# Optimization experiments

Hardware: AMD Instinct MI355X
Metric: run time of the kernel (lower is better)

## Reference

```python
import jax, jax.numpy as jnp
import numpy as np

N_NODES = 50000
N_EDGES = 800000
IN_C = 128
HID = 64
HEADS = 4
OUT_C = 32
NEG_SLOPE = 0.2
EPS = 1e-16


def _gat_conv(x, edge_index, W, att_src, att_dst, bias, heads, out_c, concat):
    # PyG GATConv (eval mode, add_self_loops=True).
    N = x.shape[0]
    # append self loops
    loops = jnp.arange(N, dtype=edge_index.dtype)
    src = jnp.concatenate([edge_index[0], loops])
    dst = jnp.concatenate([edge_index[1], loops])
    h = (x @ W).reshape(N, heads, out_c)                      # [N,H,C]
    a_src = jnp.sum(h * att_src, axis=-1)                     # [N,H]
    a_dst = jnp.sum(h * att_dst, axis=-1)                     # [N,H]
    alpha = a_src[src] + a_dst[dst]                           # [E,H]
    alpha = jnp.where(alpha >= 0, alpha, NEG_SLOPE * alpha)   # leaky_relu
    amax = jax.ops.segment_max(alpha, dst, num_segments=N)    # [N,H]
    ex = jnp.exp(alpha - amax[dst])
    denom = jax.ops.segment_sum(ex, dst, num_segments=N)      # [N,H]
    coef = ex / (denom[dst] + EPS)                            # [E,H]
    msg = h[src] * coef[:, :, None]                           # [E,H,C]
    out = jax.ops.segment_sum(msg, dst, num_segments=N)       # [N,H,C]
    if concat:
        out = out.reshape(N, heads * out_c)
    else:
        out = out.mean(axis=1)
    return out + bias


def setup_inputs() -> dict:
    key = jax.random.key(0)
    ks = jax.random.split(key, 12)
    x = jax.random.normal(ks[0], (N_NODES, IN_C), dtype=jnp.float32)
    edge_index = jax.random.randint(ks[1], (2, N_EDGES), 0, N_NODES, dtype=jnp.int64)
    s1 = 1.0 / np.sqrt(IN_C)
    s2 = 1.0 / np.sqrt(HID * HEADS)
    W1 = jax.random.uniform(ks[2], (IN_C, HEADS * HID), jnp.float32, -s1, s1)
    att_src1 = jax.random.uniform(ks[3], (HEADS, HID), jnp.float32, -s1, s1)
    att_dst1 = jax.random.uniform(ks[4], (HEADS, HID), jnp.float32, -s1, s1)
    b1 = jnp.zeros((HEADS * HID,), jnp.float32)
    W2 = jax.random.uniform(ks[5], (HEADS * HID, OUT_C), jnp.float32, -s2, s2)
    att_src2 = jax.random.uniform(ks[6], (1, OUT_C), jnp.float32, -s2, s2)
    att_dst2 = jax.random.uniform(ks[7], (1, OUT_C), jnp.float32, -s2, s2)
    b2 = jnp.zeros((OUT_C,), jnp.float32)
    return {"x": x, "edge_index": edge_index, "W1": W1, "att_src1": att_src1,
            "att_dst1": att_dst1, "b1": b1, "W2": W2, "att_src2": att_src2,
            "att_dst2": att_dst2, "b2": b2}


def reference(x, edge_index, W1, att_src1, att_dst1, b1, W2, att_src2, att_dst2, b2):
    h = _gat_conv(x, edge_index, W1, att_src1, att_dst1, b1, HEADS, HID, concat=True)
    h = jax.nn.elu(h)
    out = _gat_conv(h, edge_index, W2, att_src2, att_dst2, b2, 1, OUT_C, concat=False)
    return out
```

## Files before the change

### kernel.cpp

```cpp
#include <hip/hip_runtime.h>

#define NN 50000
#define NE 800000
#define INC 128
#define HIDC 64
#define HEADS 4
#define C1 256
#define OUTC 32
#define NEG 0.2f
#define EPSV 1e-16f
#define SLOT_CAP 56

#define NB_CASTX 3125
#define NB_ZERO  196
#define NB_W1T   128
#define NB_W2T   32
#define NB_PREP  (NB_CASTX + NB_ZERO + NB_W1T + NB_W2T)
#define EB2      3125
#define NB_G1S   782
#define NB_G1    (NB_G1S * 4)
#define NB_GS    (EB2 + NB_G1)

#define CURS  0
#define ASRC1 50000
#define ADST1 250000
#define ASRC2 450000
#define ADST2 500000
#define SLOTS 550000
#define W1T   3350000
#define W2T   3366384
#define XBF   3370480
#define H1B   6570480
#define H2B   12970480
#define H3OFF 19370480
#define WS_NEED_FLOATS 20170480ull

typedef __attribute__((ext_vector_type(8))) short short8v;
typedef __attribute__((ext_vector_type(4))) float floatx4;

__device__ __forceinline__ unsigned short f2bf(float f) {
    unsigned u = __float_as_uint(f);
    unsigned r = (u + 0x7fffu + ((u >> 16) & 1u)) >> 16;
    return (unsigned short)r;
}
__device__ __forceinline__ float bf2f(unsigned short s) {
    return __uint_as_float(((unsigned)s) << 16);
}
__device__ __forceinline__ float lrelu(float v) { return v >= 0.f ? v : NEG * v; }

__global__ __launch_bounds__(256) void prep(const float* __restrict__ x,
                                            const float* __restrict__ W1,
                                            const float* __restrict__ W2,
                                            unsigned short* __restrict__ xbf,
                                            unsigned short* __restrict__ w1t,
                                            unsigned short* __restrict__ w2t,
                                            int* __restrict__ curs) {
    const int bid = blockIdx.x, tid = threadIdx.x;
    if (bid < NB_CASTX) {
        int i = bid * 256 + tid;
        float4 v0 = ((const float4*)x)[i * 2];
        float4 v1 = ((const float4*)x)[i * 2 + 1];
        short8v o;
        o[0] = (short)f2bf(v0.x); o[1] = (short)f2bf(v0.y);
        o[2] = (short)f2bf(v0.z); o[3] = (short)f2bf(v0.w);
        o[4] = (short)f2bf(v1.x); o[5] = (short)f2bf(v1.y);
        o[6] = (short)f2bf(v1.z); o[7] = (short)f2bf(v1.w);
        *(short8v*)(xbf + (size_t)i * 8) = o;
    } else if (bid < NB_CASTX + NB_ZERO) {
        int i = (bid - NB_CASTX) * 256 + tid;
        if (i < NN) curs[i] = 0;
    } else if (bid < NB_CASTX + NB_ZERO + NB_W1T) {
        int i = (bid - NB_CASTX - NB_ZERO) * 256 + tid;
        int n = i >> 7, k = i & 127;
        w1t[(size_t)n * INC + k] = f2bf(W1[(size_t)k * C1 + n]);
    } else {
        int i = (bid - NB_CASTX - NB_ZERO - NB_W1T) * 256 + tid;
        int n = i >> 8, k = i & 255;
        w2t[(size_t)n * C1 + k] = f2bf(W2[(size_t)k * OUTC + n]);
    }
}

__global__ __launch_bounds__(256) void gemm1_scatter(const unsigned short* __restrict__ xbf,
                                                     const unsigned short* __restrict__ w1t,
                                                     const float* __restrict__ att_src,
                                                     const float* __restrict__ att_dst,
                                                     const int* __restrict__ ei,
                                                     unsigned short* __restrict__ h1b,
                                                     float* __restrict__ a_src,
                                                     float* __restrict__ a_dst,
                                                     int* __restrict__ curs,
                                                     int* __restrict__ slots) {
    const int bid = blockIdx.x;
    if (bid < EB2) {
        int e = bid * 256 + threadIdx.x;
        if (e < NE) {
            int s = ei[e], d = ei[NE + e];
            int pos = atomicAdd(&curs[d], 1);
            if (pos < SLOT_CAP) slots[(size_t)d * SLOT_CAP + pos] = s;
        }
        return;
    }
    const int b2 = bid - EB2;
    const int strip = b2 % NB_G1S;
    const int by = b2 / NB_G1S;
    const int tid = threadIdx.x;
    const int w = tid >> 6, lane = tid & 63;
    const int l15 = lane & 15, kg = lane >> 4;
    const int mb = strip * 64 + w * 16;
    const int nb = by * 64;
    int ar = mb + l15; if (ar >= NN) ar = NN - 1;

    short8v a[4];
    #pragma unroll
    for (int ks = 0; ks < 4; ++ks)
        a[ks] = *(const short8v*)(xbf + (size_t)ar * INC + ks * 32 + kg * 8);

    short8v b[4][4];
    #pragma unroll
    for (int nt = 0; nt < 4; ++nt) {
        int nc = nb + nt * 16 + l15;
        #pragma unroll
        for (int ks = 0; ks < 4; ++ks)
            b[ks][nt] = *(const short8v*)(w1t + (size_t)nc * INC + ks * 32 + kg * 8);
    }

    floatx4 acc[4] = {{0.f,0.f,0.f,0.f},{0.f,0.f,0.f,0.f},{0.f,0.f,0.f,0.f},{0.f,0.f,0.f,0.f}};
    #pragma unroll
    for (int ks = 0; ks < 4; ++ks)
        #pragma unroll
        for (int nt = 0; nt < 4; ++nt)
            acc[nt] = __builtin_amdgcn_mfma_f32_16x16x32_bf16(a[ks], b[ks][nt], acc[nt], 0, 0, 0);

    #pragma unroll
    for (int nt = 0; nt < 4; ++nt)
        #pragma unroll
        for (int j = 0; j < 4; ++j) {
            int r = mb + kg * 4 + j;
            if (r < NN) h1b[(size_t)r * C1 + nb + nt * 16 + l15] = f2bf(acc[nt][j]);
        }

    float ws_[4], wd_[4];
    #pragma unroll
    for (int nt = 0; nt < 4; ++nt) {
        ws_[nt] = att_src[nb + nt * 16 + l15];
        wd_[nt] = att_dst[nb + nt * 16 + l15];
    }
    #pragma unroll
    for (int j = 0; j < 4; ++j) {
        float ps = acc[0][j] * ws_[0] + acc[1][j] * ws_[1] + acc[2][j] * ws_[2] + acc[3][j] * ws_[3];
        float pd = acc[0][j] * wd_[0] + acc[1][j] * wd_[1] + acc[2][j] * wd_[2] + acc[3][j] * wd_[3];
        #pragma unroll
        for (int m = 8; m; m >>= 1) {
            ps += __shfl_xor(ps, m);
            pd += __shfl_xor(pd, m);
        }
        int r = mb + kg * 4 + j;
        if (l15 == 0 && r < NN) {
            a_src[r * 4 + by] = ps;
            a_dst[r * 4 + by] = pd;
        }
    }
}

__global__ __launch_bounds__(256) void node1(const unsigned short* __restrict__ h1b,
                                             const int* __restrict__ curs,
                                             const int* __restrict__ slots,
                                             const float* __restrict__ a_src,
                                             const float* __restrict__ a_dst,
                                             const float* __restrict__ b1,
                                             unsigned short* __restrict__ h2b) {
    int wave = threadIdx.x >> 6, lane = threadIdx.x & 63;
    int n = blockIdx.x * 4 + wave;
    if (n >= NN) return;
    int h = lane >> 4;
    int cnt = curs[n]; if (cnt > SLOT_CAP) cnt = SLOT_CAP;
    const int* sl = slots + (size_t)n * SLOT_CAP;
    float adh = a_dst[n * 4 + h];
    float a0 = 0.f, a1 = 0.f, a2 = 0.f, a3 = 0.f, den = 0.f;
    {
        float e = __expf(lrelu(a_src[n * 4 + h] + adh));
        den += e;
        uint2 rv = *(const uint2*)(h1b + (size_t)n * C1 + lane * 4);
        a0 += bf2f((unsigned short)(rv.x & 0xffff)) * e;
        a1 += bf2f((unsigned short)(rv.x >> 16)) * e;
        a2 += bf2f((unsigned short)(rv.y & 0xffff)) * e;
        a3 += bf2f((unsigned short)(rv.y >> 16)) * e;
    }
    int p = 0;
    for (; p + 7 < cnt; p += 8) {
        int sA[8];
        #pragma unroll
        for (int j = 0; j < 8; ++j) sA[j] = sl[p + j];
        uint2 rA[8];
        #pragma unroll
        for (int j = 0; j < 8; ++j) rA[j] = *(const uint2*)(h1b + (size_t)sA[j] * C1 + lane * 4);
        float eA[8];
        #pragma unroll
        for (int j = 0; j < 8; ++j) eA[j] = __expf(lrelu(a_src[sA[j] * 4 + h] + adh));
        #pragma unroll
        for (int j = 0; j < 8; ++j) {
            den += eA[j];
            a0 += bf2f((unsigned short)(rA[j].x & 0xffff)) * eA[j];
            a1 += bf2f((unsigned short)(rA[j].x >> 16)) * eA[j];
            a2 += bf2f((unsigned short)(rA[j].y & 0xffff)) * eA[j];
            a3 += bf2f((unsigned short)(rA[j].y >> 16)) * eA[j];
        }
    }
    for (; p + 3 < cnt; p += 4) {
        int sA[4];
        #pragma unroll
        for (int j = 0; j < 4; ++j) sA[j] = sl[p + j];
        uint2 rA[4];
        #pragma unroll
        for (int j = 0; j < 4; ++j) rA[j] = *(const uint2*)(h1b + (size_t)sA[j] * C1 + lane * 4);
        float eA[4];
        #pragma unroll
        for (int j = 0; j < 4; ++j) eA[j] = __expf(lrelu(a_src[sA[j] * 4 + h] + adh));
        #pragma unroll
        for (int j = 0; j < 4; ++j) {
            den += eA[j];
            a0 += bf2f((unsigned short)(rA[j].x & 0xffff)) * eA[j];
            a1 += bf2f((unsigned short)(rA[j].x >> 16)) * eA[j];
            a2 += bf2f((unsigned short)(rA[j].y & 0xffff)) * eA[j];
            a3 += bf2f((unsigned short)(rA[j].y >> 16)) * eA[j];
        }
    }
    for (; p < cnt; ++p) {
        int s = sl[p];
        float e = __expf(lrelu(a_src[s * 4 + h] + adh));
        den += e;
        uint2 rv = *(const uint2*)(h1b + (size_t)s * C1 + lane * 4);
        a0 += bf2f((unsigned short)(rv.x & 0xffff)) * e;
        a1 += bf2f((unsigned short)(rv.x >> 16)) * e;
        a2 += bf2f((unsigned short)(rv.y & 0xffff)) * e;
        a3 += bf2f((unsigned short)(rv.y >> 16)) * e;
    }
    float inv = 1.f / (den + EPSV);
    float4 bb = *(const float4*)(b1 + lane * 4);
    float o0 = a0 * inv + bb.x;
    float o1 = a1 * inv + bb.y;
    float o2 = a2 * inv + bb.z;
    float o3 = a3 * inv + bb.w;
    o0 = o0 > 0.f ? o0 : __expf(o0) - 1.f;
    o1 = o1 > 0.f ? o1 : __expf(o1) - 1.f;
    o2 = o2 > 0.f ? o2 : __expf(o2) - 1.f;
    o3 = o3 > 0.f ? o3 : __expf(o3) - 1.f;
    uint2 ov;
    ov.x = (unsigned)f2bf(o0) | ((unsigned)f2bf(o1) << 16);
    ov.y = (unsigned)f2bf(o2) | ((unsigned)f2bf(o3) << 16);
    *(uint2*)(h2b + (size_t)n * C1 + lane * 4) = ov;
}

__global__ __launch_bounds__(256) void gemm2_mfma(const unsigned short* __restrict__ h2b,
                                                  const unsigned short* __restrict__ w2t,
                                                  const float* __restrict__ att_src,
                                                  const float* __restrict__ att_dst,
                                                  unsigned short* __restrict__ h3b,
                                                  float* __restrict__ a_src,
                                                  float* __restrict__ a_dst) {
    const int tid = threadIdx.x;
    const int w = tid >> 6, lane = tid & 63;
    const int l15 = lane & 15, kg = lane >> 4;
    const int mb = blockIdx.x * 64 + w * 16;
    int ar = mb + l15; if (ar >= NN) ar = NN - 1;

    short8v a[8];
    #pragma unroll
    for (int ks = 0; ks < 8; ++ks)
        a[ks] = *(const short8v*)(h2b + (size_t)ar * C1 + ks * 32 + kg * 8);

    short8v b[8][2];
    #pragma unroll
    for (int nt = 0; nt < 2; ++nt) {
        int nc = nt * 16 + l15;
        #pragma unroll
        for (int ks = 0; ks < 8; ++ks)
            b[ks][nt] = *(const short8v*)(w2t + (size_t)nc * C1 + ks * 32 + kg * 8);
    }

    floatx4 acc[2] = {{0.f,0.f,0.f,0.f},{0.f,0.f,0.f,0.f}};
    #pragma unroll
    for (int ks = 0; ks < 8; ++ks)
        #pragma unroll
        for (int nt = 0; nt < 2; ++nt)
            acc[nt] = __builtin_amdgcn_mfma_f32_16x16x32_bf16(a[ks], b[ks][nt], acc[nt], 0, 0, 0);

    #pragma unroll
    for (int nt = 0; nt < 2; ++nt)
        #pragma unroll
        for (int j = 0; j < 4; ++j) {
            int r = mb + kg * 4 + j;
            if (r < NN) h3b[(size_t)r * OUTC + nt * 16 + l15] = f2bf(acc[nt][j]);
        }

    float ws0 = att_src[l15], ws1 = att_src[16 + l15];
    float wd0 = att_dst[l15], wd1 = att_dst[16 + l15];
    #pragma unroll
    for (int j = 0; j < 4; ++j) {
        float ps = acc[0][j] * ws0 + acc[1][j] * ws1;
        float pd = acc[0][j] * wd0 + acc[1][j] * wd1;
        #pragma unroll
        for (int m = 8; m; m >>= 1) {
            ps += __shfl_xor(ps, m);
            pd += __shfl_xor(pd, m);
        }
        int r = mb + kg * 4 + j;
        if (l15 == 0 && r < NN) {
            a_src[r] = ps;
            a_dst[r] = pd;
        }
    }
}

__global__ __launch_bounds__(256) void node2(const unsigned short* __restrict__ h3b,
                                             const int* __restrict__ curs,
                                             const int* __restrict__ slots,
                                             const float* __restrict__ a_src,
                                             const float* __restrict__ a_dst,
                                             const float* __restrict__ b2,
                                             float* __restrict__ out) {
    int wave = threadIdx.x >> 6, lane = threadIdx.x & 63;
    int half = lane >> 5, c = lane & 31;
    int n = blockIdx.x * 8 + wave * 2 + half;
    if (n >= NN) return;
    int cnt = curs[n]; if (cnt > SLOT_CAP) cnt = SLOT_CAP;
    const int* sl = slots + (size_t)n * SLOT_CAP;
    float adn = a_dst[n];
    float acc = 0.f, den = 0.f;
    {
        float e = __expf(lrelu(a_src[n] + adn));
        den += e;
        acc += bf2f(h3b[(size_t)n * OUTC + c]) * e;
    }
    int p = 0;
    for (; p + 3 < cnt; p += 4) {
        int s0 = sl[p], s1 = sl[p + 1], s2 = sl[p + 2], s3 = sl[p + 3];
        float g0 = bf2f(h3b[(size_t)s0 * OUTC + c]);
        float g1 = bf2f(h3b[(size_t)s1 * OUTC + c]);
        float g2 = bf2f(h3b[(size_t)s2 * OUTC + c]);
        float g3 = bf2f(h3b[(size_t)s3 * OUTC + c]);
        float e0 = __expf(lrelu(a_src[s0] + adn));
        float e1 = __expf(lrelu(a_src[s1] + adn));
        float e2 = __expf(lrelu(a_src[s2] + adn));
        float e3 = __expf(lrelu(a_src[s3] + adn));
        den += e0 + e1 + e2 + e3;
        acc += g0 * e0 + g1 * e1 + g2 * e2 + g3 * e3;
    }
    for (; p < cnt; ++p) {
        int s = sl[p];
        float e = __expf(lrelu(a_src[s] + adn));
        den += e;
        acc += bf2f(h3b[(size_t)s * OUTC + c]) * e;
    }
    out[(size_t)n * OUTC + c] = acc / (den + EPSV) + b2[c];
}

extern "C" void kernel_launch(void* const* d_in, const int* in_sizes, int n_in,
                              void* d_out, int out_size, void* d_ws, size_t ws_size,
                              hipStream_t stream) {
    if (ws_size < WS_NEED_FLOATS * 4ull) return;

    const float* x        = (const float*)d_in[0];
    const int* ei         = (const int*)d_in[1];
    const float* W1       = (const float*)d_in[2];
    const float* att_src1 = (const float*)d_in[3];
    const float* att_dst1 = (const float*)d_in[4];
    const float* b1       = (const float*)d_in[5];
    const float* W2       = (const float*)d_in[6];
    const float* att_src2 = (const float*)d_in[7];
    const float* att_dst2 = (const float*)d_in[8];
    const float* b2       = (const float*)d_in[9];
    float* out = (float*)d_out;
    float* ws  = (float*)d_ws;
    int*   wsi = (int*)d_ws;

    int*   curs   = wsi + CURS;
    float* a_src1 = ws + ASRC1;
    float* a_dst1 = ws + ADST1;
    float* a_src2 = ws + ASRC2;
    float* a_dst2 = ws + ADST2;
    int*   slots  = wsi + SLOTS;
    unsigned short* w1t = (unsigned short*)(ws + W1T);
    unsigned short* w2t = (unsigned short*)(ws + W2T);
    unsigned short* xbf = (unsigned short*)(ws + XBF);
    unsigned short* h1b = (unsigned short*)(ws + H1B);
    unsigned short* h2b = (unsigned short*)(ws + H2B);
    unsigned short* h3b = (unsigned short*)(ws + H3OFF);

    hipLaunchKernelGGL(prep, dim3(NB_PREP), dim3(256), 0, stream,
                       x, W1, W2, xbf, w1t, w2t, curs);
    hipLaunchKernelGGL(gemm1_scatter, dim3(NB_GS), dim3(256), 0, stream,
                       xbf, w1t, att_src1, att_dst1, ei, h1b, a_src1, a_dst1, curs, slots);
    hipLaunchKernelGGL(node1, dim3((NN + 3) / 4), dim3(256), 0, stream,
                       h1b, curs, slots, a_src1, a_dst1, b1, h2b);
    hipLaunchKernelGGL(gemm2_mfma, dim3((NN + 63) / 64), dim3(256), 0, stream,
                       h2b, w2t, att_src2, att_dst2, h3b, a_src2, a_dst2);
    hipLaunchKernelGGL(node2, dim3((NN + 7) / 8), dim3(256), 0, stream,
                       h3b, curs, slots, a_src2, a_dst2, b2, out);
}
```

Baseline: 199.6 us.

## Split edge scatter by destination half to overlap with node aggregation

The edge-to-slot scatter is split by destination node index. Edges into the low half are bucketed alongside the first GEMM, and edges into the high half are bucketed in a new kernel that also aggregates the low-half nodes. The high-half nodes are then aggregated in a separate kernel. The aim is to overlap scatter atomics with GEMM and aggregation work, at the cost of one extra launch and reading the edge index twice.

```diff
diff --git a/kernel.cpp b/kernel.cpp
--- a/kernel.cpp
+++ b/kernel.cpp
@@ -10,6 +10,7 @@
 #define NEG 0.2f
 #define EPSV 1e-16f
 #define SLOT_CAP 56
+#define HSPLIT 25000
 
 #define NB_CASTX 3125
 #define NB_ZERO  196
@@ -20,6 +21,8 @@
 #define NB_G1S   782
 #define NB_G1    (NB_G1S * 4)
 #define NB_GS    (EB2 + NB_G1)
+#define NB_N1H   6250
+#define NB_SN    (EB2 + NB_N1H)
 
 #define CURS  0
 #define ASRC1 50000
@@ -80,6 +83,93 @@
     }
 }
 
+__device__ __forceinline__ void node1_body(int n, int lane,
+                                           const unsigned short* __restrict__ h1b,
+                                           const int* __restrict__ curs,
+                                           const int* __restrict__ slots,
+                                           const float* __restrict__ a_src,
+                                           const float* __restrict__ a_dst,
+                                           const float* __restrict__ b1,
+                                           unsigned short* __restrict__ h2b) {
+    int h = lane >> 4;
+    int cnt = curs[n]; if (cnt > SLOT_CAP) cnt = SLOT_CAP;
+    const int* sl = slots + (size_t)n * SLOT_CAP;
+    float adh = a_dst[n * 4 + h];
+    float a0 = 0.f, a1 = 0.f, a2 = 0.f, a3 = 0.f, den = 0.f;
+    {
+        float e = __expf(lrelu(a_src[n * 4 + h] + adh));
+        den += e;
+        uint2 rv = *(const uint2*)(h1b + (size_t)n * C1 + lane * 4);
+        a0 += bf2f((unsigned short)(rv.x & 0xffff)) * e;
+        a1 += bf2f((unsigned short)(rv.x >> 16)) * e;
+        a2 += bf2f((unsigned short)(rv.y & 0xffff)) * e;
+        a3 += bf2f((unsigned short)(rv.y >> 16)) * e;
+    }
+    int p = 0;
+    for (; p + 7 < cnt; p += 8) {
+        int sA[8];
+        #pragma unroll
+        for (int j = 0; j < 8; ++j) sA[j] = sl[p + j];
+        uint2 rA[8];
+        #pragma unroll
+        for (int j = 0; j < 8; ++j) rA[j] = *(const uint2*)(h1b + (size_t)sA[j] * C1 + lane * 4);
+        float eA[8];
+        #pragma unroll
+        for (int j = 0; j < 8; ++j) eA[j] = __expf(lrelu(a_src[sA[j] * 4 + h] + adh));
+        #pragma unroll
+        for (int j = 0; j < 8; ++j) {
+            den += eA[j];
+            a0 += bf2f((unsigned short)(rA[j].x & 0xffff)) * eA[j];
+            a1 += bf2f((unsigned short)(rA[j].x >> 16)) * eA[j];
+            a2 += bf2f((unsigned short)(rA[j].y & 0xffff)) * eA[j];
+            a3 += bf2f((unsigned short)(rA[j].y >> 16)) * eA[j];
+        }
+    }
+    for (; p + 3 < cnt; p += 4) {
+        int sA[4];
+        #pragma unroll
+        for (int j = 0; j < 4; ++j) sA[j] = sl[p + j];
+        uint2 rA[4];
+        #pragma unroll
+        for (int j = 0; j < 4; ++j) rA[j] = *(const uint2*)(h1b + (size_t)sA[j] * C1 + lane * 4);
+        float eA[4];
+        #pragma unroll
+        for (int j = 0; j < 4; ++j) eA[j] = __expf(lrelu(a_src[sA[j] * 4 + h] + adh));
+        #pragma unroll
+        for (int j = 0; j < 4; ++j) {
+            den += eA[j];
+            a0 += bf2f((unsigned short)(rA[j].x & 0xffff)) * eA[j];
+            a1 += bf2f((unsigned short)(rA[j].x >> 16)) * eA[j];
+            a2 += bf2f((unsigned short)(rA[j].y & 0xffff)) * eA[j];
+            a3 += bf2f((unsigned short)(rA[j].y >> 16)) * eA[j];
+        }
+    }
+    for (; p < cnt; ++p) {
+        int s = sl[p];
+        float e = __expf(lrelu(a_src[s * 4 + h] + adh));
+        den += e;
+        uint2 rv = *(const uint2*)(h1b + (size_t)s * C1 + lane * 4);
+        a0 += bf2f((unsigned short)(rv.x & 0xffff)) * e;
+        a1 += bf2f((unsigned short)(rv.x >> 16)) * e;
+        a2 += bf2f((unsigned short)(rv.y & 0xffff)) * e;
+        a3 += bf2f((unsigned short)(rv.y >> 16)) * e;
+    }
+    float inv = 1.f / (den + EPSV);
+    float4 bb = *(const float4*)(b1 + lane * 4);
+    float o0 = a0 * inv + bb.x;
+    float o1 = a1 * inv + bb.y;
+    float o2 = a2 * inv + bb.z;
+    float o3 = a3 * inv + bb.w;
+    o0 = o0 > 0.f ? o0 : __expf(o0) - 1.f;
+    o1 = o1 > 0.f ? o1 : __expf(o1) - 1.f;
+    o2 = o2 > 0.f ? o2 : __expf(o2) - 1.f;
+    o3 = o3 > 0.f ? o3 : __expf(o3) - 1.f;
+    uint2 ov;
+    ov.x = (unsigned)f2bf(o0) | ((unsigned)f2bf(o1) << 16);
+    ov.y = (unsigned)f2bf(o2) | ((unsigned)f2bf(o3) << 16);
+    *(uint2*)(h2b + (size_t)n * C1 + lane * 4) = ov;
+}
+
 __global__ __launch_bounds__(256) void gemm1_scatter(const unsigned short* __restrict__ xbf,
                                                      const unsigned short* __restrict__ w1t,
                                                      const float* __restrict__ att_src,
@@ -94,9 +184,12 @@
     if (bid < EB2) {
         int e = bid * 256 + threadIdx.x;
         if (e < NE) {
-            int s = ei[e], d = ei[NE + e];
-            int pos = atomicAdd(&curs[d], 1);
-            if (pos < SLOT_CAP) slots[(size_t)d * SLOT_CAP + pos] = s;
+            int d = ei[NE + e];
+            if (d < HSPLIT) {
+                int s = ei[e];
+                int pos = atomicAdd(&curs[d], 1);
+                if (pos < SLOT_CAP) slots[(size_t)d * SLOT_CAP + pos] = s;
+            }
         }
         return;
     }
@@ -162,93 +255,44 @@
     }
 }
 
-__global__ __launch_bounds__(256) void node1(const unsigned short* __restrict__ h1b,
-                                             const int* __restrict__ curs,
-                                             const int* __restrict__ slots,
-                                             const float* __restrict__ a_src,
-                                             const float* __restrict__ a_dst,
-                                             const float* __restrict__ b1,
-                                             unsigned short* __restrict__ h2b) {
+__global__ __launch_bounds__(256) void scatter_node1(const int* __restrict__ ei,
+                                                     const unsigned short* __restrict__ h1b,
+                                                     const float* __restrict__ a_src,
+                                                     const float* __restrict__ a_dst,
+                                                     const float* __restrict__ b1,
+                                                     int* __restrict__ curs,
+                                                     int* __restrict__ slots,
+                                                     unsigned short* __restrict__ h2b) {
+    const int bid = blockIdx.x;
+    if (bid < EB2) {
+        int e = bid * 256 + threadIdx.x;
+        if (e < NE) {
+            int d = ei[NE + e];
+            if (d >= HSPLIT) {
+                int s = ei[e];
+                int pos = atomicAdd(&curs[d], 1);
+                if (pos < SLOT_CAP) slots[(size_t)d * SLOT_CAP + pos] = s;
+            }
+        }
+        return;
+    }
     int wave = threadIdx.x >> 6, lane = threadIdx.x & 63;
-    int n = blockIdx.x * 4 + wave;
+    int n = (bid - EB2) * 4 + wave;
+    if (n >= HSPLIT) return;
+    node1_body(n, lane, h1b, curs, slots, a_src, a_dst, b1, h2b);
+}
+
+__global__ __launch_bounds__(256) void node1_hi(const unsigned short* __restrict__ h1b,
+                                                const int* __restrict__ curs,
+                                                const int* __restrict__ slots,
+                                                const float* __restrict__ a_src,
+                                                const float* __restrict__ a_dst,
+                                                const float* __restrict__ b1,
+                                                unsigned short* __restrict__ h2b) {
+    int wave = threadIdx.x >> 6, lane = threadIdx.x & 63;
+    int n = HSPLIT + blockIdx.x * 4 + wave;
     if (n >= NN) return;
-    int h = lane >> 4;
-    int cnt = curs[n]; if (cnt > SLOT_CAP) cnt = SLOT_CAP;
-    const int* sl = slots + (size_t)n * SLOT_CAP;
-    float adh = a_dst[n * 4 + h];
-    float a0 = 0.f, a1 = 0.f, a2 = 0.f, a3 = 0.f, den = 0.f;
-    {
-        float e = __expf(lrelu(a_src[n * 4 + h] + adh));
-        den += e;
-        uint2 rv = *(const uint2*)(h1b + (size_t)n * C1 + lane * 4);
-        a0 += bf2f((unsigned short)(rv.x & 0xffff)) * e;
-        a1 += bf2f((unsigned short)(rv.x >> 16)) * e;
-        a2 += bf2f((unsigned short)(rv.y & 0xffff)) * e;
-        a3 += bf2f((unsigned short)(rv.y >> 16)) * e;
-    }
-    int p = 0;
-    for (; p + 7 < cnt; p += 8) {
-        int sA[8];
-        #pragma unroll
-        for (int j = 0; j < 8; ++j) sA[j] = sl[p + j];
-        uint2 rA[8];
-        #pragma unroll
-        for (int j = 0; j < 8; ++j) rA[j] = *(const uint2*)(h1b + (size_t)sA[j] * C1 + lane * 4);
-        float eA[8];
-        #pragma unroll
-        for (int j = 0; j < 8; ++j) eA[j] = __expf(lrelu(a_src[sA[j] * 4 + h] + adh));
-        #pragma unroll
-        for (int j = 0; j < 8; ++j) {
-            den += eA[j];
-            a0 += bf2f((unsigned short)(rA[j].x & 0xffff)) * eA[j];
-            a1 += bf2f((unsigned short)(rA[j].x >> 16)) * eA[j];
-            a2 += bf2f((unsigned short)(rA[j].y & 0xffff)) * eA[j];
-            a3 += bf2f((unsigned short)(rA[j].y >> 16)) * eA[j];
-        }
-    }
-    for (; p + 3 < cnt; p += 4) {
-        int sA[4];
-        #pragma unroll
-        for (int j = 0; j < 4; ++j) sA[j] = sl[p + j];
-        uint2 rA[4];
-        #pragma unroll
-        for (int j = 0; j < 4; ++j) rA[j] = *(const uint2*)(h1b + (size_t)sA[j] * C1 + lane * 4);
-        float eA[4];
-        #pragma unroll
-        for (int j = 0; j < 4; ++j) eA[j] = __expf(lrelu(a_src[sA[j] * 4 + h] + adh));
-        #pragma unroll
-        for (int j = 0; j < 4; ++j) {
-            den += eA[j];
-            a0 += bf2f((unsigned short)(rA[j].x & 0xffff)) * eA[j];
-            a1 += bf2f((unsigned short)(rA[j].x >> 16)) * eA[j];
-            a2 += bf2f((unsigned short)(rA[j].y & 0xffff)) * eA[j];
-            a3 += bf2f((unsigned short)(rA[j].y >> 16)) * eA[j];
-        }
-    }
-    for (; p < cnt; ++p) {
-        int s = sl[p];
-        float e = __expf(lrelu(a_src[s * 4 + h] + adh));
-        den += e;
-        uint2 rv = *(const uint2*)(h1b + (size_t)s * C1 + lane * 4);
-        a0 += bf2f((unsigned short)(rv.x & 0xffff)) * e;
-        a1 += bf2f((unsigned short)(rv.x >> 16)) * e;
-        a2 += bf2f((unsigned short)(rv.y & 0xffff)) * e;
-        a3 += bf2f((unsigned short)(rv.y >> 16)) * e;
-    }
-    float inv = 1.f / (den + EPSV);
-    float4 bb = *(const float4*)(b1 + lane * 4);
-    float o0 = a0 * inv + bb.x;
-    float o1 = a1 * inv + bb.y;
-    float o2 = a2 * inv + bb.z;
-    float o3 = a3 * inv + bb.w;
-    o0 = o0 > 0.f ? o0 : __expf(o0) - 1.f;
-    o1 = o1 > 0.f ? o1 : __expf(o1) - 1.f;
-    o2 = o2 > 0.f ? o2 : __expf(o2) - 1.f;
-    o3 = o3 > 0.f ? o3 : __expf(o3) - 1.f;
-    uint2 ov;
-    ov.x = (unsigned)f2bf(o0) | ((unsigned)f2bf(o1) << 16);
-    ov.y = (unsigned)f2bf(o2) | ((unsigned)f2bf(o3) << 16);
-    *(uint2*)(h2b + (size_t)n * C1 + lane * 4) = ov;
+    node1_body(n, lane, h1b, curs, slots, a_src, a_dst, b1, h2b);
 }
 
 __global__ __launch_bounds__(256) void gemm2_mfma(const unsigned short* __restrict__ h2b,
@@ -391,7 +435,9 @@
                        x, W1, W2, xbf, w1t, w2t, curs);
     hipLaunchKernelGGL(gemm1_scatter, dim3(NB_GS), dim3(256), 0, stream,
                        xbf, w1t, att_src1, att_dst1, ei, h1b, a_src1, a_dst1, curs, slots);
-    hipLaunchKernelGGL(node1, dim3((NN + 3) / 4), dim3(256), 0, stream,
+    hipLaunchKernelGGL(scatter_node1, dim3(NB_SN), dim3(256), 0, stream,
+                       ei, h1b, a_src1, a_dst1, b1, curs, slots, h2b);
+    hipLaunchKernelGGL(node1_hi, dim3(NB_N1H), dim3(256), 0, stream,
                        h1b, curs, slots, a_src1, a_dst1, b1, h2b);
     hipLaunchKernelGGL(gemm2_mfma, dim3((NN + 63) / 64), dim3(256), 0, stream,
                        h2b, w2t, att_src2, att_dst2, h3b, a_src2, a_dst2);
```

Result: slower. 207.0 us (+3.7%).
